# Performance work log

Measured on AMD Instinct MI355X. Metric: run time of the kernel, lower is better.

The kernel has to match this reference:

```python
import jax, jax.numpy as jnp
import numpy as np

NUM_BINS = 256  # must be > max input value (fill_max)

def setup_inputs() -> dict:
    key = jax.random.key(0)
    inputs = jax.random.randint(key, (128, 256, 32, 32), 0, NUM_BINS, dtype=jnp.int32)
    return {"inputs": inputs}

def reference(inputs) -> jnp.ndarray:
    # Faithful to tf: reshape [B,P,S,S] -> [B, P*S*S] (tf.math.bincount flattens
    # its per-map_fn 2D input), per-batch-element histogram, max bin count.
    B = inputs.shape[0]
    flat = inputs.reshape(B, -1)  # [B, N]

    def hist_max(row):
        counts = jnp.zeros((NUM_BINS,), dtype=jnp.int32).at[row].add(1)
        return jnp.max(counts)

    out = jax.vmap(hist_max)(flat)  # [B] int32: mode frequency per batch element
    return out.astype(jnp.float32)
```

## Files before the change

kernel.cpp:

```cpp
#include <hip/hip_runtime.h>
#include <hip/hip_bf16.h>


#define NUM_BINS 256
#define NREP     32
#define BPB      4
#define N_PER_B  (256 * 32 * 32)
#define CHUNK    (N_PER_B / BPB)
#define BLOCK1   1024

__global__ __launch_bounds__(BLOCK1) void
percolation_hist_kernel(const int* __restrict__ in, int* __restrict__ part) {
    __shared__ int lh[NUM_BINS * NREP];

    for (int i = threadIdx.x; i < NUM_BINS * NREP; i += BLOCK1)
        lh[i] = 0;
    __syncthreads();

    const int lane = threadIdx.x & (NREP - 1);

    const int4* p = (const int4*)(in + (size_t)blockIdx.x * CHUNK);
    const int iters = CHUNK / 4 / BLOCK1;

#pragma unroll 4
    for (int i = 0; i < iters; ++i) {
        int4 v = p[(size_t)i * BLOCK1 + threadIdx.x];
        atomicAdd(&lh[v.x * NREP + lane], 1);
        atomicAdd(&lh[v.y * NREP + lane], 1);
        atomicAdd(&lh[v.z * NREP + lane], 1);
        atomicAdd(&lh[v.w * NREP + lane], 1);
    }
    __syncthreads();

    if (threadIdx.x < NUM_BINS) {
        int s = 0;
#pragma unroll
        for (int j = 0; j < NREP; ++j)
            s += lh[threadIdx.x * NREP + ((j + threadIdx.x) & (NREP - 1))];
        part[blockIdx.x * NUM_BINS + threadIdx.x] = s;
    }
}

__global__ __launch_bounds__(NUM_BINS) void
percolation_max_kernel(const int* __restrict__ part, float* __restrict__ out) {
    const int batch = blockIdx.x;
    const int bin   = threadIdx.x;

    const int* p = part + (size_t)batch * BPB * NUM_BINS;
    int v = 0;
#pragma unroll
    for (int s = 0; s < BPB; ++s)
        v += p[s * NUM_BINS + bin];

#pragma unroll
    for (int off = 32; off > 0; off >>= 1)
        v = max(v, __shfl_down(v, off, 64));

    __shared__ int wmax[NUM_BINS / 64];
    if ((threadIdx.x & 63) == 0)
        wmax[threadIdx.x >> 6] = v;
    __syncthreads();

    if (threadIdx.x == 0) {
        int m = wmax[0];
#pragma unroll
        for (int w = 1; w < NUM_BINS / 64; ++w)
            m = max(m, wmax[w]);
        out[batch] = (float)m;
    }
}

extern "C" void kernel_launch(void* const* d_in, const int* in_sizes, int n_in,
                              void* d_out, int out_size, void* d_ws, size_t ws_size,
                              hipStream_t stream) {
    const int* in   = (const int*)d_in[0];
    float*     out  = (float*)d_out;
    int*       part = (int*)d_ws;

    const int B = out_size;

    percolation_hist_kernel<<<B * BPB, BLOCK1, 0, stream>>>(in, part);
    percolation_max_kernel<<<B, NUM_BINS, 0, stream>>>(part, out);
}
```

Baseline: 187.8 us.

## Fuse histogram and max into one kernel with one block per batch

Each block now processes an entire batch element's histogram and computes the max bin count in place, removing the partial-histogram workspace and the second kernel launch. The grid shrinks from 512 to 128 blocks, which on a GPU with many CUs leaves most CUs idle and cuts memory-level parallelism for this bandwidth-heavy read. The unroll factor also rises from 4 to 8.

```diff
diff --git a/kernel.cpp b/kernel.cpp
--- a/kernel.cpp
+++ b/kernel.cpp
@@ -1,30 +1,27 @@
 #include <hip/hip_runtime.h>
-#include <hip/hip_bf16.h>
 
 
 #define NUM_BINS 256
 #define NREP     32
-#define BPB      4
+#define BLOCK    1024
 #define N_PER_B  (256 * 32 * 32)
-#define CHUNK    (N_PER_B / BPB)
-#define BLOCK1   1024
 
-__global__ __launch_bounds__(BLOCK1) void
-percolation_hist_kernel(const int* __restrict__ in, int* __restrict__ part) {
+__global__ __launch_bounds__(BLOCK) void
+percolation_fused_kernel(const int* __restrict__ in, float* __restrict__ out) {
     __shared__ int lh[NUM_BINS * NREP];
 
-    for (int i = threadIdx.x; i < NUM_BINS * NREP; i += BLOCK1)
+    for (int i = threadIdx.x; i < NUM_BINS * NREP; i += BLOCK)
         lh[i] = 0;
     __syncthreads();
 
     const int lane = threadIdx.x & (NREP - 1);
 
-    const int4* p = (const int4*)(in + (size_t)blockIdx.x * CHUNK);
-    const int iters = CHUNK / 4 / BLOCK1;
+    const int4* p = (const int4*)(in + (size_t)blockIdx.x * N_PER_B);
+    const int iters = N_PER_B / 4 / BLOCK;
 
-#pragma unroll 4
+#pragma unroll 8
     for (int i = 0; i < iters; ++i) {
-        int4 v = p[(size_t)i * BLOCK1 + threadIdx.x];
+        int4 v = p[(size_t)i * BLOCK + threadIdx.x];
         atomicAdd(&lh[v.x * NREP + lane], 1);
         atomicAdd(&lh[v.y * NREP + lane], 1);
         atomicAdd(&lh[v.z * NREP + lane], 1);
@@ -32,53 +29,37 @@
     }
     __syncthreads();
 
+    int s = 0;
     if (threadIdx.x < NUM_BINS) {
-        int s = 0;
 #pragma unroll
         for (int j = 0; j < NREP; ++j)
             s += lh[threadIdx.x * NREP + ((j + threadIdx.x) & (NREP - 1))];
-        part[blockIdx.x * NUM_BINS + threadIdx.x] = s;
     }
-}
-
-__global__ __launch_bounds__(NUM_BINS) void
-percolation_max_kernel(const int* __restrict__ part, float* __restrict__ out) {
-    const int batch = blockIdx.x;
-    const int bin   = threadIdx.x;
-
-    const int* p = part + (size_t)batch * BPB * NUM_BINS;
-    int v = 0;
-#pragma unroll
-    for (int s = 0; s < BPB; ++s)
-        v += p[s * NUM_BINS + bin];
 
 #pragma unroll
     for (int off = 32; off > 0; off >>= 1)
-        v = max(v, __shfl_down(v, off, 64));
+        s = max(s, __shfl_down(s, off, 64));
 
-    __shared__ int wmax[NUM_BINS / 64];
+    __shared__ int wmax[BLOCK / 64];
     if ((threadIdx.x & 63) == 0)
-        wmax[threadIdx.x >> 6] = v;
+        wmax[threadIdx.x >> 6] = s;
     __syncthreads();
 
     if (threadIdx.x == 0) {
         int m = wmax[0];
 #pragma unroll
-        for (int w = 1; w < NUM_BINS / 64; ++w)
+        for (int w = 1; w < BLOCK / 64; ++w)
             m = max(m, wmax[w]);
-        out[batch] = (float)m;
+        out[blockIdx.x] = (float)m;
     }
 }
 
 extern "C" void kernel_launch(void* const* d_in, const int* in_sizes, int n_in,
                               void* d_out, int out_size, void* d_ws, size_t ws_size,
                               hipStream_t stream) {
-    const int* in   = (const int*)d_in[0];
-    float*     out  = (float*)d_out;
-    int*       part = (int*)d_ws;
-
+    const int* in  = (const int*)d_in[0];
+    float*     out = (float*)d_out;
     const int B = out_size;
 
-    percolation_hist_kernel<<<B * BPB, BLOCK1, 0, stream>>>(in, part);
-    percolation_max_kernel<<<B, NUM_BINS, 0, stream>>>(part, out);
+    percolation_fused_kernel<<<B, BLOCK, 0, stream>>>(in, out);
 }
```

Result: slower. 195.8 us (+4.3%).
